# Kernel optimization log

Hardware: AMD Instinct MI355X
Metric: run time of the kernel (lower is better)

The kernel has to match this reference:

```python
import jax, jax.numpy as jnp
import numpy as np

# ---- geometry / filter constants (from source script) ----
N0, N1, N2 = 16, 200, 200
NUM_RAD, NUM_PHI = 223, 190
VOX = 2.0                      # mm, isotropic voxel size
STEP = 2.0                     # mm, ray sampling step
SCAN_R = 350.0                 # scanner radius -> rays span [-350, 350] mm
NUM_T = int(2 * SCAN_R / STEP) + 1   # 351 samples per ray
SIGMA = 4.5 / (2.35 * VOX)     # gaussian sigma in voxels
RADIUS = int(4.0 * SIGMA + 0.5)      # scipy truncate=4 convention
ORG1 = (-N1 / 2 + 0.5) * VOX
ORG2 = (-N2 / 2 + 0.5) * VOX

_phis = np.linspace(0.0, np.pi, NUM_PHI, endpoint=False, dtype=np.float32)
COS = jnp.asarray(np.cos(_phis), dtype=jnp.float32)
SIN = jnp.asarray(np.sin(_phis), dtype=jnp.float32)
RV = jnp.asarray(np.linspace(-200.0, 200.0, NUM_RAD, dtype=np.float32))
TV = jnp.asarray(np.linspace(-SCAN_R, SCAN_R, NUM_T, dtype=np.float32))
_g = np.exp(-0.5 * (np.arange(-RADIUS, RADIUS + 1) / SIGMA) ** 2)
GW = jnp.asarray((_g / _g.sum()).astype(np.float32))


def _smooth_axis(x, axis):
    pad = [(0, 0)] * x.ndim
    pad[axis] = (RADIUS, RADIUS)
    xp = jnp.pad(x, pad, mode='symmetric')
    n = x.shape[axis]
    return sum(GW[k] * jax.lax.slice_in_dim(xp, k, k + n, axis=axis)
               for k in range(2 * RADIUS + 1))


def gauss3(x):
    # separable 3D gaussian (GaussianFilterOperator)
    for ax in range(3):
        x = _smooth_axis(x, ax)
    return x


def _bilinear(img, ix, iy):
    # img [n0, n1, n2]; ix/iy [num_rad, num_t] fractional voxel coords
    i0 = jnp.floor(ix); j0 = jnp.floor(iy)
    fi = ix - i0; fj = iy - j0
    i0 = i0.astype(jnp.int32); j0 = j0.astype(jnp.int32)
    valid = ((ix >= 0) & (ix <= N1 - 1) & (iy >= 0) & (iy <= N2 - 1)).astype(img.dtype)
    i0c = jnp.clip(i0, 0, N1 - 1); i1c = jnp.clip(i0 + 1, 0, N1 - 1)
    j0c = jnp.clip(j0, 0, N2 - 1); j1c = jnp.clip(j0 + 1, 0, N2 - 1)
    v = ((1 - fi) * (1 - fj) * img[:, i0c, j0c]
         + fi * (1 - fj) * img[:, i1c, j0c]
         + (1 - fi) * fj * img[:, i0c, j1c]
         + fi * fj * img[:, i1c, j1c])          # [n0, num_rad, num_t]
    return v * valid


def project(img):
    # ParallelViewProjector2D: line integrals per slice -> [n0, num_phi, num_rad]
    def body(_, cs):
        c, s = cs
        # ray point = r * perp(phi) + t * dir(phi); perp=(-s,c), dir=(c,s)
        ix = (RV[:, None] * (-s) + TV[None, :] * c - ORG1) / VOX
        iy = (RV[:, None] * c + TV[None, :] * s - ORG2) / VOX
        return None, _bilinear(img, ix, iy).sum(-1) * STEP
    _, sino = jax.lax.scan(body, None, (COS, SIN))   # [num_phi, n0, num_rad]
    return jnp.transpose(sino, (1, 0, 2))


def fwd_model(x, mult):
    # CompositeLinearOperator((sens_mult, projector, gaussian_filter))
    return mult * project(gauss3(x))


def adjoint_model(y, mult, like):
    # exact adjoint of the linear fwd_model via vjp
    _, vjpf = jax.vjp(lambda u: fwd_model(u, mult), jnp.zeros_like(like))
    return vjpf(y)[0]


def setup_inputs() -> dict:
    key = jax.random.key(0)
    k1, k2, k3, k4 = jax.random.split(key, 4)
    x = jax.random.uniform(k1, (N0, N1, N2), dtype=jnp.float32) + 0.1
    data = jax.random.uniform(k2, (N0, NUM_PHI, NUM_RAD), dtype=jnp.float32) * 10.0
    contamination = jax.random.uniform(k3, (N0, NUM_PHI, NUM_RAD), dtype=jnp.float32) * 0.5 + 0.5
    mult = jax.random.uniform(k4, (N0, NUM_PHI, NUM_RAD), dtype=jnp.float32) * 0.5 + 0.5
    ones_sino = jnp.ones((N0, NUM_PHI, NUM_RAD), dtype=jnp.float32)
    sens_image = jnp.maximum(adjoint_model(ones_sino, mult, x), 1e-2)
    return {"x": x, "data": data, "contamination": contamination,
            "mult": mult, "sens_image": sens_image}


def reference(x, data, contamination, mult, sens_image):
    # PoissonEMModule.forward: one MLEM update
    exp = fwd_model(x, mult) + contamination
    return x * adjoint_model(data / exp, mult, x) / sens_image
```

## Files before the change

### kernel.cpp

```cpp
#include <hip/hip_runtime.h>
#include <math.h>

#define N0 16
#define N1 200
#define N2 200
#define NPIX (N1 * N2)
#define NVOX (N0 * NPIX)
#define NUM_RAD 223
#define NUM_PHI 190
#define NUM_T 351
#define NSINO (N0 * NUM_PHI * NUM_RAD)
#define PITCH16 3328
#define S16 (3328 * 210)
#define BASEOFF16 (4 * 3328 + 4 * 16)
#define BP_CHUNK 38
#define BP_NCH 5

__global__ void init_consts(float* __restrict__ cosb, float* __restrict__ sinb,
                            float* __restrict__ rvb, float* __restrict__ gwb) {
    int t = threadIdx.x;
    const double PI = 3.14159265358979311599796346854418516159;
    if (t < NUM_PHI) {
        double step = PI / 190.0;
        float phif = (float)((double)t * step);
        cosb[t] = (float)cos((double)phif);
        sinb[t] = (float)sin((double)phif);
    }
    if (t < NUM_RAD) {
        double step = 400.0 / 222.0;
        float rv = (float)(-200.0 + (double)t * step);
        if (t == NUM_RAD - 1) rv = 200.0f;
        rvb[t] = rv;
    }
    if (t == 0) {
        double sig = 4.5 / (2.35 * 2.0);
        double g[9], ssum = 0.0;
        for (int k = 0; k < 9; ++k) { double d = (double)(k - 4) / sig; g[k] = exp(-0.5 * d * d); ssum += g[k]; }
        for (int k = 0; k < 9; ++k) gwb[k] = (float)(g[k] / ssum);
    }
}

__global__ void smooth_fwd(const float* __restrict__ in, float* __restrict__ out,
                           const float* __restrict__ gwb, int n, int stride) {
    int e = blockIdx.x * 256 + threadIdx.x;
    if (e >= NVOX) return;
    int a = (e / stride) % n;
    int base = e - a * stride;
    float sum = 0.f;
#pragma unroll
    for (int k = 0; k < 9; ++k) {
        int q = a + k - 4;
        q = (q < 0) ? (-1 - q) : ((q >= n) ? (2 * n - 1 - q) : q);
        sum = __fadd_rn(sum, __fmul_rn(gwb[k], in[base + q * stride]));
    }
    out[e] = sum;
}

__global__ void smooth_fwd2_16(const float* __restrict__ in, float* __restrict__ P16,
                               float* __restrict__ PT16, const float* __restrict__ gwb) {
    int t = blockIdx.x * 256 + threadIdx.x;
    if (t >= 2 * NPIX) return;
    int oct = t & 1;
    int pix = t >> 1;
    int i1 = pix / N2;
    int i2 = pix - i1 * N2;
    int rowbase = i1 * N2;
    float v[8];
#pragma unroll
    for (int jj = 0; jj < 8; ++jj) {
        int i0 = oct * 8 + jj;
        const float* tin = in + i0 * NPIX + rowbase;
        float sum = 0.f;
#pragma unroll
        for (int k = 0; k < 9; ++k) {
            int q = i2 + k - 4;
            q = (q < 0) ? (-1 - q) : ((q >= N2) ? (2 * N2 - 1 - q) : q);
            sum = __fadd_rn(sum, __fmul_rn(gwb[k], tin[q]));
        }
        v[jj] = sum;
    }
    int po  = BASEOFF16 + i1 * PITCH16 + i2 * 16 + oct * 8;
    int pto = BASEOFF16 + i2 * PITCH16 + i1 * 16 + oct * 8;
    *(float4*)(P16 + po)      = make_float4(v[0], v[1], v[2], v[3]);
    *(float4*)(P16 + po + 4)  = make_float4(v[4], v[5], v[6], v[7]);
    *(float4*)(PT16 + pto)     = make_float4(v[0], v[1], v[2], v[3]);
    *(float4*)(PT16 + pto + 4) = make_float4(v[4], v[5], v[6], v[7]);
}

__device__ __forceinline__ float adj_u(const float* __restrict__ in, const float* __restrict__ gwb,
                                       int base, int stride, int n, int j) {
    float r = 0.f;
#pragma unroll
    for (int k = 0; k < 9; ++k) {
        int i = j - k;
        if (i >= 0 && i < n) r = __fadd_rn(r, __fmul_rn(gwb[k], in[base + i * stride]));
    }
    return r;
}

__global__ void smooth_adj(const float* __restrict__ in, float* __restrict__ out,
                           const float* __restrict__ gwb, int n, int stride) {
    int e = blockIdx.x * 256 + threadIdx.x;
    if (e >= NVOX) return;
    int a = (e / stride) % n;
    int base = e - a * stride;
    float v = adj_u(in, gwb, base, stride, n, a + 4);
    if (a < 4)      v = __fadd_rn(v, adj_u(in, gwb, base, stride, n, 3 - a));
    if (a >= n - 4) v = __fadd_rn(v, adj_u(in, gwb, base, stride, n, 2 * n + 3 - a));
    out[e] = v;
}

__device__ __forceinline__ float sum5_at(const float* __restrict__ a, const float* __restrict__ b,
                                         const float* __restrict__ c, const float* __restrict__ d,
                                         const float* __restrict__ e5, int i) {
    return __fadd_rn(__fadd_rn(__fadd_rn(a[i], b[i]), __fadd_rn(c[i], d[i])), e5[i]);
}

__device__ __forceinline__ float adj_u5(const float* __restrict__ a, const float* __restrict__ b,
                                        const float* __restrict__ c, const float* __restrict__ d,
                                        const float* __restrict__ e5, const float* __restrict__ gwb,
                                        int base, int n, int j) {
    float r = 0.f;
#pragma unroll
    for (int k = 0; k < 9; ++k) {
        int i = j - k;
        if (i >= 0 && i < n) r = __fadd_rn(r, __fmul_rn(gwb[k], sum5_at(a, b, c, d, e5, base + i)));
    }
    return r;
}

__global__ void smooth_adj2_sum5(const float* __restrict__ a, const float* __restrict__ b,
                                 const float* __restrict__ c, const float* __restrict__ d,
                                 const float* __restrict__ e5, const float* __restrict__ gwb,
                                 float* __restrict__ out) {
    int e = blockIdx.x * 256 + threadIdx.x;
    if (e >= NVOX) return;
    int i2 = e % N2;
    int base = e - i2;
    float v = adj_u5(a, b, c, d, e5, gwb, base, N2, i2 + 4);
    if (i2 < 4)       v = __fadd_rn(v, adj_u5(a, b, c, d, e5, gwb, base, N2, 3 - i2));
    if (i2 >= N2 - 4) v = __fadd_rn(v, adj_u5(a, b, c, d, e5, gwb, base, N2, 2 * N2 + 3 - i2));
    out[e] = v;
}

__global__ void smooth_adj0_final(const float* __restrict__ in, const float* __restrict__ x,
                                  const float* __restrict__ sens, const float* __restrict__ gwb,
                                  float* __restrict__ out) {
    int e = blockIdx.x * 256 + threadIdx.x;
    if (e >= NVOX) return;
    int a = e / NPIX;
    int base = e - a * NPIX;
    float v = adj_u(in, gwb, base, NPIX, N0, a + 4);
    if (a < 4)  v = __fadd_rn(v, adj_u(in, gwb, base, NPIX, N0, 3 - a));
    if (a >= 12) v = __fadd_rn(v, adj_u(in, gwb, base, NPIX, N0, 35 - a));
    out[e] = __fdiv_rn(__fmul_rn(x[e], v), sens[e]);
}

template<bool USET>
__device__ __forceinline__ void geom2(float tv, float ch, float sh, float Ah, float Bh,
                                      float& w00, float& w10, float& w01, float& w11,
                                      int& o) {
    float ix = fmaf(tv, ch, Ah);
    float iy = fmaf(tv, sh, Bh);
    bool valid = (ix >= 0.f) & (ix <= 199.f) & (iy >= 0.f) & (iy <= 199.f);
    float fx = floorf(ix), fy = floorf(iy);
    int ii = (int)fx, jj = (int)fy;
    float fi = ix - fx, fj = iy - fy;
    int rowi = USET ? jj : ii;
    int coli = USET ? ii : jj;
    o = rowi * PITCH16 + coli * 16;
    float gi = 1.f - fi, gj = 1.f - fj;
    w00 = valid ? gi * gj : 0.f;
    w10 = valid ? fi * gj : 0.f;
    w01 = valid ? gi * fj : 0.f;
    w11 = valid ? fi * fj : 0.f;
}

#define CONSUME4(W00, W10, W01, W11, V00, V10, V01, V11)                         \
    sums[0] = fmaf(W00, V00.x, sums[0]); sums[0] = fmaf(W10, V10.x, sums[0]);    \
    sums[0] = fmaf(W01, V01.x, sums[0]); sums[0] = fmaf(W11, V11.x, sums[0]);    \
    sums[1] = fmaf(W00, V00.y, sums[1]); sums[1] = fmaf(W10, V10.y, sums[1]);    \
    sums[1] = fmaf(W01, V01.y, sums[1]); sums[1] = fmaf(W11, V11.y, sums[1]);    \
    sums[2] = fmaf(W00, V00.z, sums[2]); sums[2] = fmaf(W10, V10.z, sums[2]);    \
    sums[2] = fmaf(W01, V01.z, sums[2]); sums[2] = fmaf(W11, V11.z, sums[2]);    \
    sums[3] = fmaf(W00, V00.w, sums[3]); sums[3] = fmaf(W10, V10.w, sums[3]);    \
    sums[3] = fmaf(W01, V01.w, sums[3]); sums[3] = fmaf(W11, V11.w, sums[3]);

#define LOADB(DST00, DST10, DST01, DST11, OFF)                                   \
    DST00 = *(const float4*)(basep + (OFF));                                     \
    DST10 = *(const float4*)(basep + (OFF) + O10);                               \
    DST01 = *(const float4*)(basep + (OFF) + O01);                               \
    DST11 = *(const float4*)(basep + (OFF) + O10 + O01);

template<bool USET>
__device__ __forceinline__ void ray_loop(const float* __restrict__ basep,
                                         int kbeg, int kend, float ch, float sh,
                                         float Ah, float Bh, float sums[4]) {
    constexpr int O10 = USET ? 16 : PITCH16;
    constexpr int O01 = USET ? PITCH16 : 16;
    float tv = (float)(2 * kbeg - 350);
    float aw00, aw10, aw01, aw11; int ao;
    geom2<USET>(tv, ch, sh, Ah, Bh, aw00, aw10, aw01, aw11, ao);
    float4 A00, A10, A01, A11;
    LOADB(A00, A10, A01, A11, ao);
    if (kbeg == kend) {
        CONSUME4(aw00, aw10, aw01, aw11, A00, A10, A01, A11);
        return;
    }
    float bw00, bw10, bw01, bw11; int bo;
    tv += 2.0f;
    geom2<USET>(tv, ch, sh, Ah, Bh, bw00, bw10, bw01, bw11, bo);
    float4 B00, B10, B01, B11;
    LOADB(B00, B10, B01, B11, bo);
    int k = kbeg;
#pragma unroll 1
    while (k + 3 <= kend) {
        CONSUME4(aw00, aw10, aw01, aw11, A00, A10, A01, A11);
        tv += 2.0f;
        geom2<USET>(tv, ch, sh, Ah, Bh, aw00, aw10, aw01, aw11, ao);
        LOADB(A00, A10, A01, A11, ao);
        CONSUME4(bw00, bw10, bw01, bw11, B00, B10, B01, B11);
        tv += 2.0f;
        geom2<USET>(tv, ch, sh, Ah, Bh, bw00, bw10, bw01, bw11, bo);
        LOADB(B00, B10, B01, B11, bo);
        k += 2;
    }
    if (kend == k + 1) {
        CONSUME4(aw00, aw10, aw01, aw11, A00, A10, A01, A11);
        CONSUME4(bw00, bw10, bw01, bw11, B00, B10, B01, B11);
    } else {
        CONSUME4(aw00, aw10, aw01, aw11, A00, A10, A01, A11);
        tv += 2.0f;
        geom2<USET>(tv, ch, sh, Ah, Bh, aw00, aw10, aw01, aw11, ao);
        LOADB(A00, A10, A01, A11, ao);
        CONSUME4(bw00, bw10, bw01, bw11, B00, B10, B01, B11);
        CONSUME4(aw00, aw10, aw01, aw11, A00, A10, A01, A11);
    }
}

__global__ __launch_bounds__(512, 2)
void project_ratio(const float* __restrict__ P16, const float* __restrict__ PT16,
                   const float* __restrict__ data,
                   const float* __restrict__ contam, const float* __restrict__ mult,
                   const float* __restrict__ cosb, const float* __restrict__ sinb,
                   const float* __restrict__ rvb, float* __restrict__ zt) {
    int b = blockIdx.x;
    int sw = (b & 7) * 95 + (b >> 3);
    int rc  = sw / NUM_PHI;
    int phi = sw - rc * NUM_PHI;
    int tx = threadIdx.x;
    int chunk = tx & 3;
    int rr = tx >> 2;
    int r = rc * 64 + rr;
    int half = threadIdx.y;
    bool active = (r < NUM_RAD);

    __shared__ float part[4][256];

    float sums[4] = {0.f, 0.f, 0.f, 0.f};
    float c = cosb[phi], sp = sinb[phi];
    float ch = c * 0.5f, sh = sp * 0.5f;

    bool useT = fabsf(sp) > fabsf(c);
    const float* basep = (useT ? PT16 : P16) + BASEOFF16 + chunk * 4;

    if (active) {
        float rv = rvb[r];
        float A = __fmul_rn(rv, -sp);
        float B = __fmul_rn(rv, c);
        float Ah = fmaf(rv, -sh, 99.5f);
        float Bh = fmaf(rv, ch, 99.5f);

        float tlo = -350.f, thi = 350.f;
        bool empty = false;
        if (fabsf(c) > 1e-6f) {
            float a0 = (-199.f - A) / c, b0 = (199.f - A) / c;
            tlo = fmaxf(tlo, fminf(a0, b0)); thi = fminf(thi, fmaxf(a0, b0));
        } else if (fabsf(A) > 199.5f) empty = true;
        if (fabsf(sp) > 1e-6f) {
            float a0 = (-199.f - B) / sp, b0 = (199.f - B) / sp;
            tlo = fmaxf(tlo, fminf(a0, b0)); thi = fminf(thi, fmaxf(a0, b0));
        } else if (fabsf(B) > 199.5f) empty = true;

        int klo = max(0, (int)floorf((tlo + 350.f) * 0.5f) - 1);
        int khi = min(NUM_T - 1, (int)ceilf((thi + 350.f) * 0.5f) + 1);

        if (!empty && klo <= khi) {
            int kmid = (klo + khi + 1) >> 1;
            int kbeg = half ? kmid : klo;
            int kend = half ? khi : (kmid - 1);
            if (kbeg <= kend) {
                if (useT) ray_loop<true>(basep, kbeg, kend, ch, sh, Ah, Bh, sums);
                else      ray_loop<false>(basep, kbeg, kend, ch, sh, Ah, Bh, sums);
            }
        }
    }

    if (half == 1) {
#pragma unroll
        for (int s = 0; s < 4; ++s) part[s][tx] = sums[s];
    }
    __syncthreads();
    if (half == 0 && active) {
#pragma unroll
        for (int s = 0; s < 4; ++s) {
            float proj = __fmul_rn(__fadd_rn(sums[s], part[s][tx]), 2.0f);
            int sl = chunk * 4 + s;
            int idx = (sl * NUM_PHI + phi) * NUM_RAD + r;
            float ex = __fadd_rn(__fmul_rn(mult[idx], proj), contam[idx]);
            float zval = __fmul_rn(mult[idx], __fdiv_rn(data[idx], ex));
            zt[(phi * NUM_RAD + r) * N0 + sl] = zval;
        }
    }
}

__global__ __launch_bounds__(256, 6)
void backproject(const float* __restrict__ zt, const float* __restrict__ cosb,
                 const float* __restrict__ sinb, const float* __restrict__ rvb,
                 float* __restrict__ q0, float* __restrict__ q1, float* __restrict__ q2,
                 float* __restrict__ q3, float* __restrict__ q4) {
    int tx = threadIdx.x;
    int q = tx & 3;
    int pix = blockIdx.x * 64 + (tx >> 2);
    int pc = blockIdx.y;
    int i1 = pix / N2;
    int i2 = pix - i1 * N2;
    float X1 = 2.f * (float)i1 - 199.f;
    float X2 = 2.f * (float)i2 - 199.f;
    float i1f = (float)i1, i2f = (float)i2;
    int lb = tx & 60;
    float acc[4] = {0.f, 0.f, 0.f, 0.f};

    int p_end = pc * BP_CHUNK + BP_CHUNK;
    for (int p = pc * BP_CHUNK; p < p_end; ++p) {
        float c = cosb[p], sp = sinb[p];
        float ch = c * 0.5f, sh = sp * 0.5f;
        float tp = c * X1 + sp * X2;
        float rp = c * X2 - sp * X1;
        int j0 = (int)floorf((rp + 200.f) * 0.555f);
        int jb = min(max(j0 - 1, 0), NUM_RAD - 4);
        float tc = (tp + 350.f) * 0.5f;
        int kc = (int)floorf(tc + 0.5f);

        const float4* zb = (const float4*)(zt + (p * NUM_RAD + jb) * N0);
        float4 Z0 = zb[q];
        float4 Z1 = zb[4 + q];
        float4 Z2 = zb[8 + q];
        float4 Z3 = zb[12 + q];

        float tvc = (float)(2 * kc - 350);
        float Qx[3], Qy[3];
#pragma unroll
        for (int dk = 0; dk < 3; ++dk) {
            float tv = tvc + (float)(2 * (dk - 1));
            Qx[dk] = fmaf(tv, ch, 99.5f);
            Qy[dk] = fmaf(tv, sh, 99.5f);
        }
        float rvj = rvb[jb + q];
        float Px = rvj * (-sh);
        float Py = rvj * ch;
        float w = 0.f;
#pragma unroll
        for (int dk = 0; dk < 3; ++dk) {
            float ix = Px + Qx[dk];
            float iy = Py + Qy[dk];
            bool valid = (ix >= 0.f) & (ix <= 199.f) & (iy >= 0.f) & (iy <= 199.f);
            float wx = fmaxf(0.f, 1.f - fabsf(ix - i1f));
            float wy = fmaxf(0.f, 1.f - fabsf(iy - i2f));
            float wxm = valid ? wx : 0.f;
            w = fmaf(wxm, wy, w);
        }

        float w0 = __shfl(w, lb + 0);
        float w1 = __shfl(w, lb + 1);
        float w2 = __shfl(w, lb + 2);
        float w3 = __shfl(w, lb + 3);

        acc[0] = fmaf(w0, Z0.x, acc[0]); acc[1] = fmaf(w0, Z0.y, acc[1]);
        acc[2] = fmaf(w0, Z0.z, acc[2]); acc[3] = fmaf(w0, Z0.w, acc[3]);
        acc[0] = fmaf(w1, Z1.x, acc[0]); acc[1] = fmaf(w1, Z1.y, acc[1]);
        acc[2] = fmaf(w1, Z1.z, acc[2]); acc[3] = fmaf(w1, Z1.w, acc[3]);
        acc[0] = fmaf(w2, Z2.x, acc[0]); acc[1] = fmaf(w2, Z2.y, acc[1]);
        acc[2] = fmaf(w2, Z2.z, acc[2]); acc[3] = fmaf(w2, Z2.w, acc[3]);
        acc[0] = fmaf(w3, Z3.x, acc[0]); acc[1] = fmaf(w3, Z3.y, acc[1]);
        acc[2] = fmaf(w3, Z3.z, acc[2]); acc[3] = fmaf(w3, Z3.w, acc[3]);
    }

    float* pp = (pc == 0) ? q0 : (pc == 1) ? q1 : (pc == 2) ? q2 : (pc == 3) ? q3 : q4;
#pragma unroll
    for (int i = 0; i < 4; ++i)
        pp[(q * 4 + i) * NPIX + pix] = acc[i] * 2.0f;
}

extern "C" void kernel_launch(void* const* d_in, const int* in_sizes, int n_in,
                              void* d_out, int out_size, void* d_ws, size_t ws_size,
                              hipStream_t stream) {
    const float* x      = (const float*)d_in[0];
    const float* data   = (const float*)d_in[1];
    const float* contam = (const float*)d_in[2];
    const float* mult   = (const float*)d_in[3];
    const float* sens   = (const float*)d_in[4];
    float* out = (float*)d_out;

    float* W    = (float*)d_ws;
    float* s    = W;
    float* tmp  = W + NVOX;
    float* bp2  = W + 2 * NVOX;
    float* zt   = W + 3 * NVOX;
    float* P16  = W + 3 * NVOX + NSINO;
    float* PT16 = P16 + S16;
    float* cosb = PT16 + S16;
    float* sinb = cosb + NUM_PHI;
    float* rvb  = sinb + NUM_PHI;
    float* gwb  = rvb + NUM_RAD;

    hipLaunchKernelGGL(init_consts, dim3(1), dim3(256), 0, stream, cosb, sinb, rvb, gwb);

    int nb = (NVOX + 255) / 256;
    hipLaunchKernelGGL(smooth_fwd, dim3(nb), dim3(256), 0, stream, x,   s,   gwb, N0, NPIX);
    hipLaunchKernelGGL(smooth_fwd, dim3(nb), dim3(256), 0, stream, s,   tmp, gwb, N1, N2);
    int nb2 = (2 * NPIX + 255) / 256;
    hipLaunchKernelGGL(smooth_fwd2_16, dim3(nb2), dim3(256), 0, stream, tmp, P16, PT16, gwb);

    hipLaunchKernelGGL(project_ratio, dim3(NUM_PHI * 4), dim3(256, 2), 0, stream,
                       P16, PT16, data, contam, mult, cosb, sinb, rvb, zt);

    hipLaunchKernelGGL(backproject, dim3(NPIX / 64, BP_NCH), dim3(256), 0, stream,
                       zt, cosb, sinb, rvb, s, tmp, bp2, P16, PT16);

    hipLaunchKernelGGL(smooth_adj2_sum5, dim3(nb), dim3(256), 0, stream,
                       s, tmp, bp2, P16, PT16, gwb, zt);
    hipLaunchKernelGGL(smooth_adj, dim3(nb), dim3(256), 0, stream, zt, s, gwb, N1, N2);
    hipLaunchKernelGGL(smooth_adj0_final, dim3(nb), dim3(256), 0, stream, s, x, sens, gwb, out);
}
```

Before: 260.4 us.

## Fuse first two forward smoothing passes and deepen projector sample pipeline to three

Replaces the two separate axis-0 and axis-1 Gaussian passes with one kernel that computes the 9x9 two-axis convolution directly from x, removing one launch and one full-volume intermediate write and read. The price is 81 loads per output instead of 18, which rely on cache hits. Separately, the ray-marching helper in the projector now keeps three bilinear sample loads in flight instead of two, to hide more memory latency. This costs extra registers under the 512-thread, 2-block launch bounds and adds a more complex tail.

```diff
diff --git a/kernel.cpp b/kernel.cpp
--- a/kernel.cpp
+++ b/kernel.cpp
@@ -40,20 +40,34 @@
     }
 }
 
-__global__ void smooth_fwd(const float* __restrict__ in, float* __restrict__ out,
-                           const float* __restrict__ gwb, int n, int stride) {
+__global__ void smooth_fwd01(const float* __restrict__ x, float* __restrict__ out,
+                             const float* __restrict__ gwb) {
     int e = blockIdx.x * 256 + threadIdx.x;
     if (e >= NVOX) return;
-    int a = (e / stride) % n;
-    int base = e - a * stride;
-    float sum = 0.f;
+    int i0 = e / NPIX;
+    int rem = e - i0 * NPIX;
+    int i1 = rem / N2;
+    int i2 = rem - i1 * N2;
+    int off0[9];
 #pragma unroll
     for (int k = 0; k < 9; ++k) {
-        int q = a + k - 4;
-        q = (q < 0) ? (-1 - q) : ((q >= n) ? (2 * n - 1 - q) : q);
-        sum = __fadd_rn(sum, __fmul_rn(gwb[k], in[base + q * stride]));
-    }
-    out[e] = sum;
+        int q = i0 + k - 4;
+        q = (q < 0) ? (-1 - q) : ((q >= N0) ? (2 * N0 - 1 - q) : q);
+        off0[k] = q * NPIX;
+    }
+    float outv = 0.f;
+#pragma unroll
+    for (int k1 = 0; k1 < 9; ++k1) {
+        int q1 = i1 + k1 - 4;
+        q1 = (q1 < 0) ? (-1 - q1) : ((q1 >= N1) ? (2 * N1 - 1 - q1) : q1);
+        int base = q1 * N2 + i2;
+        float sv = 0.f;
+#pragma unroll
+        for (int k0 = 0; k0 < 9; ++k0)
+            sv = __fadd_rn(sv, __fmul_rn(gwb[k0], x[off0[k0] + base]));
+        outv = __fadd_rn(outv, __fmul_rn(gwb[k1], sv));
+    }
+    out[e] = outv;
 }
 
 __global__ void smooth_fwd2_16(const float* __restrict__ in, float* __restrict__ P16,
@@ -212,9 +226,19 @@
     geom2<USET>(tv, ch, sh, Ah, Bh, bw00, bw10, bw01, bw11, bo);
     float4 B00, B10, B01, B11;
     LOADB(B00, B10, B01, B11, bo);
+    if (kbeg + 1 == kend) {
+        CONSUME4(aw00, aw10, aw01, aw11, A00, A10, A01, A11);
+        CONSUME4(bw00, bw10, bw01, bw11, B00, B10, B01, B11);
+        return;
+    }
+    float cw00, cw10, cw01, cw11; int co;
+    tv += 2.0f;
+    geom2<USET>(tv, ch, sh, Ah, Bh, cw00, cw10, cw01, cw11, co);
+    float4 C00, C10, C01, C11;
+    LOADB(C00, C10, C01, C11, co);
     int k = kbeg;
 #pragma unroll 1
-    while (k + 3 <= kend) {
+    while (k + 5 <= kend) {
         CONSUME4(aw00, aw10, aw01, aw11, A00, A10, A01, A11);
         tv += 2.0f;
         geom2<USET>(tv, ch, sh, Ah, Bh, aw00, aw10, aw01, aw11, ao);
@@ -223,19 +247,28 @@
         tv += 2.0f;
         geom2<USET>(tv, ch, sh, Ah, Bh, bw00, bw10, bw01, bw11, bo);
         LOADB(B00, B10, B01, B11, bo);
-        k += 2;
-    }
-    if (kend == k + 1) {
-        CONSUME4(aw00, aw10, aw01, aw11, A00, A10, A01, A11);
-        CONSUME4(bw00, bw10, bw01, bw11, B00, B10, B01, B11);
-    } else {
-        CONSUME4(aw00, aw10, aw01, aw11, A00, A10, A01, A11);
+        CONSUME4(cw00, cw10, cw01, cw11, C00, C10, C01, C11);
+        tv += 2.0f;
+        geom2<USET>(tv, ch, sh, Ah, Bh, cw00, cw10, cw01, cw11, co);
+        LOADB(C00, C10, C01, C11, co);
+        k += 3;
+    }
+    int rem = kend - k;
+    CONSUME4(aw00, aw10, aw01, aw11, A00, A10, A01, A11);
+    if (rem >= 3) {
         tv += 2.0f;
         geom2<USET>(tv, ch, sh, Ah, Bh, aw00, aw10, aw01, aw11, ao);
         LOADB(A00, A10, A01, A11, ao);
-        CONSUME4(bw00, bw10, bw01, bw11, B00, B10, B01, B11);
-        CONSUME4(aw00, aw10, aw01, aw11, A00, A10, A01, A11);
-    }
+    }
+    CONSUME4(bw00, bw10, bw01, bw11, B00, B10, B01, B11);
+    if (rem == 4) {
+        tv += 2.0f;
+        geom2<USET>(tv, ch, sh, Ah, Bh, bw00, bw10, bw01, bw11, bo);
+        LOADB(B00, B10, B01, B11, bo);
+    }
+    CONSUME4(cw00, cw10, cw01, cw11, C00, C10, C01, C11);
+    if (rem >= 3) { CONSUME4(aw00, aw10, aw01, aw11, A00, A10, A01, A11); }
+    if (rem == 4) { CONSUME4(bw00, bw10, bw01, bw11, B00, B10, B01, B11); }
 }
 
 __global__ __launch_bounds__(512, 2)
@@ -417,8 +450,7 @@
     hipLaunchKernelGGL(init_consts, dim3(1), dim3(256), 0, stream, cosb, sinb, rvb, gwb);
 
     int nb = (NVOX + 255) / 256;
-    hipLaunchKernelGGL(smooth_fwd, dim3(nb), dim3(256), 0, stream, x,   s,   gwb, N0, NPIX);
-    hipLaunchKernelGGL(smooth_fwd, dim3(nb), dim3(256), 0, stream, s,   tmp, gwb, N1, N2);
+    hipLaunchKernelGGL(smooth_fwd01, dim3(nb), dim3(256), 0, stream, x, tmp, gwb);
     int nb2 = (2 * NPIX + 255) / 256;
     hipLaunchKernelGGL(smooth_fwd2_16, dim3(nb2), dim3(256), 0, stream, tmp, P16, PT16, gwb);
 
```

Result: no change. 263.8 us (+1.3%).
